# Optimization experiments

Measured on AMD Instinct MI355X. Metric: run time of the kernel, lower is better.

The kernel has to match this reference:

```python
import jax, jax.numpy as jnp
import numpy as np
from jax import lax

T, IMG, C_IN = 2048, 84, 4
HID = 256
NUM_OUT = 18
FEAT = 6 * 6 * 32  # 84 -> 42 -> 21 -> 11 -> 6 with stride-2 SAME convs


def setup_inputs() -> dict:
    key = jax.random.key(0)
    ks = jax.random.split(key, 8)
    d = {}
    d["x"] = jax.random.normal(ks[0], (T, IMG, IMG, C_IN), jnp.float32)
    cin = C_IN
    for i in range(4):
        d[f"conv_w{i}"] = jax.random.normal(ks[1 + i], (3, 3, cin, 32), jnp.float32) * (1.0 / np.sqrt(9 * cin))
        d[f"conv_b{i}"] = jnp.zeros((32,), jnp.float32)
        cin = 32
    d["lstm_w"] = jax.random.normal(ks[5], (FEAT + HID, 4 * HID), jnp.float32) * (1.0 / np.sqrt(FEAT + HID))
    d["lstm_b"] = jnp.zeros((4 * HID,), jnp.float32)
    d["fc_w"] = jax.random.normal(ks[6], (HID, NUM_OUT), jnp.float32) * 0.01
    d["fc_b"] = jnp.zeros((NUM_OUT,), jnp.float32)
    d["c_in"] = jnp.zeros((1, HID), jnp.float32)
    d["h_in"] = jnp.zeros((1, HID), jnp.float32)
    return d


def _conv_stack(x, ws, bs):
    dn = ("NHWC", "HWIO", "NHWC")
    for w, b in zip(ws, bs):
        x = jax.nn.elu(lax.conv_general_dilated(x, w, (2, 2), "SAME", dimension_numbers=dn) + b)
    return x.reshape(x.shape[0], -1)  # [T, FEAT]


def _lstm(feats, c0, h0, lstm_w, lstm_b):
    # BasicLSTMCell: gates [i, j, f, o], forget_bias = 1.0
    def step(carry, xt):
        c, h = carry  # [1, HID] each
        z = jnp.concatenate([xt[None, :], h], axis=1) @ lstm_w + lstm_b
        i, j, f, o = jnp.split(z, 4, axis=1)
        c = c * jax.nn.sigmoid(f + 1.0) + jax.nn.sigmoid(i) * jnp.tanh(j)
        h = jnp.tanh(c) * jax.nn.sigmoid(o)
        return (c, h), h[0]

    (_, _), hs = lax.scan(step, (c0, h0), feats)
    return hs  # [T, HID]


def reference(x, c_in, h_in,
              conv_w0, conv_b0, conv_w1, conv_b1,
              conv_w2, conv_b2, conv_w3, conv_b3,
              lstm_w, lstm_b, fc_w, fc_b):
    feats = _conv_stack(x, [conv_w0, conv_w1, conv_w2, conv_w3],
                        [conv_b0, conv_b1, conv_b2, conv_b3])
    hs = _lstm(feats, c_in, h_in, lstm_w, lstm_b)
    logits = hs @ fc_w + fc_b  # [T, NUM_OUT]
    return logits, hs
```

## Files before the change

kernel.cpp:

```cpp
#include <hip/hip_runtime.h>
#include <hip/hip_bf16.h>

__device__ inline float fsig(float x) { return 1.0f / (1.0f + __expf(-x)); }
__device__ inline float ftanh(float x) {
    float ax = fabsf(x);
    float e = __expf(-2.0f * ax);
    float r = (1.0f - e) / (1.0f + e);
    return x >= 0.0f ? r : -r;
}
__device__ inline float felu(float x) { return x > 0.0f ? x : expm1f(x); }

typedef _Float16 h2_t __attribute__((ext_vector_type(2)));

__device__ inline unsigned int packh2(float a, float b) {
    unsigned short ua = __builtin_bit_cast(unsigned short, (_Float16)a);
    unsigned short ub = __builtin_bit_cast(unsigned short, (_Float16)b);
    return (unsigned int)ua | ((unsigned int)ub << 16);
}
__device__ inline unsigned short f16bits(float a) {
    return __builtin_bit_cast(unsigned short, (_Float16)a);
}

__device__ inline float dot2acc(unsigned int w, unsigned int h, float acc) {
#if __has_builtin(__builtin_amdgcn_fdot2)
    return __builtin_amdgcn_fdot2(__builtin_bit_cast(h2_t, w), __builtin_bit_cast(h2_t, h), acc, false);
#else
    _Float16 wlo = __builtin_bit_cast(_Float16, (unsigned short)(w & 0xffff));
    _Float16 whi = __builtin_bit_cast(_Float16, (unsigned short)(w >> 16));
    _Float16 hlo = __builtin_bit_cast(_Float16, (unsigned short)(h & 0xffff));
    _Float16 hhi = __builtin_bit_cast(_Float16, (unsigned short)(h >> 16));
    return acc + (float)wlo * (float)hlo + (float)whi * (float)hhi;
#endif
}

template <int CIN, int W, int OW, int PAD>
__global__ __launch_bounds__(256) void conv_row(const float* __restrict__ in,
                                                const float* __restrict__ wg,
                                                const float* __restrict__ bias,
                                                float* __restrict__ out) {
    constexpr int WP = W + 2;
    __shared__ float in_s[3 * WP * CIN];
    constexpr int NQ = 3 * WP * CIN / 4;
    constexpr int QROW = WP * CIN / 4;
    const int tid = threadIdx.x;
    const int oy = blockIdx.x;
    const int t = blockIdx.y;
    const int co = tid & 31;

    for (int q = tid; q < NQ; q += 256) {
        int ky = q / QROW;
        int rem = q - ky * QROW;
        int col = rem / (CIN / 4);
        int c4 = rem - col * (CIN / 4);
        int iy = 2 * oy - PAD + ky;
        int ix = col - 1;
        float4 v = make_float4(0.f, 0.f, 0.f, 0.f);
        if (iy >= 0 && iy < W && ix >= 0 && ix < W)
            v = *(const float4*)&in[(((size_t)t * W + iy) * W + ix) * CIN + c4 * 4];
        *(float4*)&in_s[q * 4] = v;
    }

    if constexpr (CIN == 4) {
        float wr[9][4];
#pragma unroll
        for (int tap = 0; tap < 9; ++tap)
#pragma unroll
            for (int j = 0; j < 4; ++j) wr[tap][j] = wg[(tap * 4 + j) * 32 + co];
        __syncthreads();

        const int g = tid >> 5;
        constexpr int NOX = (OW + 7) / 8;
        float acc[NOX];
#pragma unroll
        for (int m = 0; m < NOX; ++m) acc[m] = 0.f;
#pragma unroll
        for (int ky = 0; ky < 3; ++ky)
#pragma unroll
            for (int kx = 0; kx < 3; ++kx) {
                float w0 = wr[ky * 3 + kx][0], w1 = wr[ky * 3 + kx][1];
                float w2 = wr[ky * 3 + kx][2], w3 = wr[ky * 3 + kx][3];
#pragma unroll
                for (int m = 0; m < NOX; ++m) {
                    int ox = g + 8 * m;
                    if (ox < OW) {
                        int cs = 2 * ox + kx - PAD + 1;
                        float4 xi = *(const float4*)&in_s[(ky * WP + cs) * 4];
                        acc[m] += xi.x * w0 + xi.y * w1 + xi.z * w2 + xi.w * w3;
                    }
                }
            }
        float b = bias[co];
#pragma unroll
        for (int m = 0; m < NOX; ++m) {
            int ox = g + 8 * m;
            if (ox < OW)
                out[(((size_t)t * OW + oy) * OW + ox) * 32 + co] = felu(acc[m] + b);
        }
    } else {
        const int cig = tid >> 5;
        float wr[9][4];
#pragma unroll
        for (int tap = 0; tap < 9; ++tap)
#pragma unroll
            for (int j = 0; j < 4; ++j) wr[tap][j] = wg[(tap * 32 + cig * 4 + j) * 32 + co];
        __syncthreads();

        float acc[OW];
#pragma unroll
        for (int ox = 0; ox < OW; ++ox) acc[ox] = 0.f;
#pragma unroll
        for (int ky = 0; ky < 3; ++ky)
#pragma unroll
            for (int kx = 0; kx < 3; ++kx) {
                const float* ip = &in_s[(ky * WP) * 32 + cig * 4];
                float w0 = wr[ky * 3 + kx][0], w1 = wr[ky * 3 + kx][1];
                float w2 = wr[ky * 3 + kx][2], w3 = wr[ky * 3 + kx][3];
#pragma unroll
                for (int ox = 0; ox < OW; ++ox) {
                    int cs = 2 * ox + kx - PAD + 1;
                    float4 xi = *(const float4*)&ip[cs * 32];
                    acc[ox] += xi.x * w0 + xi.y * w1 + xi.z * w2 + xi.w * w3;
                }
            }
        __shared__ float zs[8][OW * 32];
#pragma unroll
        for (int ox = 0; ox < OW; ++ox) zs[cig][ox * 32 + co] = acc[ox];
        __syncthreads();
        for (int idx = tid; idx < OW * 32; idx += 256) {
            float s = zs[0][idx] + zs[1][idx] + zs[2][idx] + zs[3][idx] +
                      zs[4][idx] + zs[5][idx] + zs[6][idx] + zs[7][idx] + bias[idx & 31];
            out[(((size_t)t * OW + oy) * OW) * 32 + idx] = felu(s);
        }
    }
}

__global__ void gemm_kernel(const float* __restrict__ A, const float* __restrict__ Wx,
                            const float* __restrict__ bias, float* __restrict__ C) {
    __shared__ float As[32][64];
    __shared__ float Bs[32][64];
    const int bn = blockIdx.x, bm = blockIdx.y;
    const int tx = threadIdx.x, ty = threadIdx.y;
    const int tid = ty * 16 + tx;
    float acc[4][4] = {};
    for (int k0 = 0; k0 < 1152; k0 += 32) {
        {
            int r = tid >> 3;
            int c = (tid & 7) * 4;
            float4 a0 = *(const float4*)&A[(size_t)(bm * 64 + r) * 1152 + k0 + c];
            float4 a1 = *(const float4*)&A[(size_t)(bm * 64 + r + 32) * 1152 + k0 + c];
            As[c + 0][r] = a0.x; As[c + 1][r] = a0.y; As[c + 2][r] = a0.z; As[c + 3][r] = a0.w;
            As[c + 0][r + 32] = a1.x; As[c + 1][r + 32] = a1.y; As[c + 2][r + 32] = a1.z; As[c + 3][r + 32] = a1.w;
            int rb = tid >> 4;
            int cb = (tid & 15) * 4;
            *(float4*)&Bs[rb][cb] = *(const float4*)&Wx[(size_t)(k0 + rb) * 1024 + bn * 64 + cb];
            *(float4*)&Bs[rb + 16][cb] = *(const float4*)&Wx[(size_t)(k0 + rb + 16) * 1024 + bn * 64 + cb];
        }
        __syncthreads();
#pragma unroll
        for (int kk = 0; kk < 32; ++kk) {
            float4 a = *(float4*)&As[kk][ty * 4];
            float4 b = *(float4*)&Bs[kk][tx * 4];
            acc[0][0] += a.x * b.x; acc[0][1] += a.x * b.y; acc[0][2] += a.x * b.z; acc[0][3] += a.x * b.w;
            acc[1][0] += a.y * b.x; acc[1][1] += a.y * b.y; acc[1][2] += a.y * b.z; acc[1][3] += a.y * b.w;
            acc[2][0] += a.z * b.x; acc[2][1] += a.z * b.y; acc[2][2] += a.z * b.z; acc[2][3] += a.z * b.w;
            acc[3][0] += a.w * b.x; acc[3][1] += a.w * b.y; acc[3][2] += a.w * b.z; acc[3][3] += a.w * b.w;
        }
        __syncthreads();
    }
#pragma unroll
    for (int i = 0; i < 4; ++i) {
        int row = bm * 64 + ty * 4 + i;
#pragma unroll
        for (int j = 0; j < 4; ++j) {
            int col = bn * 64 + tx * 4 + j;
            C[(size_t)row * 1024 + col] = acc[i][j] + bias[col];
        }
    }
}

__global__ __launch_bounds__(512, 2) void lstm4_kernel(const float* __restrict__ lstm_w,
                                                       const float* __restrict__ xpart,
                                                       const float* __restrict__ c_in,
                                                       const float* __restrict__ h_in,
                                                       float* __restrict__ hs_out) {
    __shared__ __align__(16) unsigned int wlds[1024][36];
    __shared__ float zsm[1024];
    __shared__ __align__(16) unsigned short hbuf[2][256];

    const int tid = threadIdx.x;
    const int c0 = tid;
    const int c1 = tid + 512;

    for (int p = 0; p < 32; ++p) {
        wlds[c0][p] = packh2(lstm_w[(size_t)(1152 + 2 * p) * 1024 + c0],
                             lstm_w[(size_t)(1152 + 2 * p + 1) * 1024 + c0]);
        wlds[c1][p] = packh2(lstm_w[(size_t)(1152 + 2 * p) * 1024 + c1],
                             lstm_w[(size_t)(1152 + 2 * p + 1) * 1024 + c1]);
    }
    unsigned int wrA[96], wrB[96];
#pragma unroll
    for (int r = 0; r < 96; ++r) {
        int p = 32 + r;
        wrA[r] = packh2(lstm_w[(size_t)(1152 + 2 * p) * 1024 + c0],
                        lstm_w[(size_t)(1152 + 2 * p + 1) * 1024 + c0]);
        wrB[r] = packh2(lstm_w[(size_t)(1152 + 2 * p) * 1024 + c1],
                        lstm_w[(size_t)(1152 + 2 * p + 1) * 1024 + c1]);
    }

    float c_state = 0.0f;
    if (tid < 256) {
        c_state = c_in[tid];
        hbuf[0][tid] = f16bits(h_in[tid]);
    }
    __syncthreads();

    float xpA = xpart[c0];
    float xpB = xpart[c1];
    for (int t = 0; t < 2048; ++t) {
        const int cur = t & 1;
        const uint4* hq = reinterpret_cast<const uint4*>(&hbuf[cur][0]);

        float a0 = 0.f, a1 = 0.f, a2 = 0.f, a3 = 0.f;
        float b0 = 0.f, b1 = 0.f, b2 = 0.f, b3 = 0.f;
#pragma unroll
        for (int c = 0; c < 8; ++c) {
            uint4 h4 = hq[c];
            uint4 wa = *reinterpret_cast<const uint4*>(&wlds[c0][4 * c]);
            uint4 wb = *reinterpret_cast<const uint4*>(&wlds[c1][4 * c]);
            a0 = dot2acc(wa.x, h4.x, a0); a1 = dot2acc(wa.y, h4.y, a1);
            a2 = dot2acc(wa.z, h4.z, a2); a3 = dot2acc(wa.w, h4.w, a3);
            b0 = dot2acc(wb.x, h4.x, b0); b1 = dot2acc(wb.y, h4.y, b1);
            b2 = dot2acc(wb.z, h4.z, b2); b3 = dot2acc(wb.w, h4.w, b3);
        }
#pragma unroll
        for (int c = 8; c < 32; ++c) {
            uint4 h4 = hq[c];
            const int r = 4 * c - 32;
            a0 = dot2acc(wrA[r + 0], h4.x, a0); a1 = dot2acc(wrA[r + 1], h4.y, a1);
            a2 = dot2acc(wrA[r + 2], h4.z, a2); a3 = dot2acc(wrA[r + 3], h4.w, a3);
            b0 = dot2acc(wrB[r + 0], h4.x, b0); b1 = dot2acc(wrB[r + 1], h4.y, b1);
            b2 = dot2acc(wrB[r + 2], h4.z, b2); b3 = dot2acc(wrB[r + 3], h4.w, b3);
        }
        zsm[c0] = (a0 + a1) + (a2 + a3) + xpA;
        zsm[c1] = (b0 + b1) + (b2 + b3) + xpB;

        float xpAn = 0.f, xpBn = 0.f;
        if (t + 1 < 2048) {
            xpAn = xpart[(size_t)(t + 1) * 1024 + c0];
            xpBn = xpart[(size_t)(t + 1) * 1024 + c1];
        }

        asm volatile("s_waitcnt lgkmcnt(0)\n\ts_barrier" ::: "memory");

        if (tid < 256) {
            float zi = zsm[tid];
            float zg = zsm[256 + tid];
            float zf = zsm[512 + tid];
            float zo = zsm[768 + tid];
            c_state = c_state * fsig(zf + 1.0f) + fsig(zi) * ftanh(zg);
            float h = ftanh(c_state) * fsig(zo);
            hs_out[(size_t)t * 256 + tid] = h;
            hbuf[cur ^ 1][tid] = f16bits(h);
        }

        asm volatile("s_waitcnt lgkmcnt(0)\n\ts_barrier" ::: "memory");
        xpA = xpAn;
        xpB = xpBn;
    }
}

__global__ void logits_kernel(const float* __restrict__ hs, const float* __restrict__ fc_w,
                              const float* __restrict__ fc_b, float* __restrict__ out) {
    int idx = blockIdx.x * 256 + threadIdx.x;
    if (idx >= 2048 * 18) return;
    int t = idx / 18, n = idx % 18;
    float acc = fc_b[n];
    const float* hrow = hs + (size_t)t * 256;
#pragma unroll 4
    for (int k = 0; k < 256; ++k) acc += hrow[k] * fc_w[k * 18 + n];
    out[idx] = acc;
}

extern "C" void kernel_launch(void* const* d_in, const int* in_sizes, int n_in,
                              void* d_out, int out_size, void* d_ws, size_t ws_size,
                              hipStream_t stream) {
    const float* x   = (const float*)d_in[0];
    const float* w0  = (const float*)d_in[1];
    const float* b0  = (const float*)d_in[2];
    const float* w1  = (const float*)d_in[3];
    const float* b1  = (const float*)d_in[4];
    const float* w2  = (const float*)d_in[5];
    const float* b2  = (const float*)d_in[6];
    const float* w3  = (const float*)d_in[7];
    const float* b3  = (const float*)d_in[8];
    const float* lw  = (const float*)d_in[9];
    const float* lb  = (const float*)d_in[10];
    const float* fcw = (const float*)d_in[11];
    const float* fcb = (const float*)d_in[12];
    const float* cin = (const float*)d_in[13];
    const float* hin = (const float*)d_in[14];

    float* outp = (float*)d_out;
    float* hs_out = outp + 2048 * 18;

    const size_t PERT = 56448 + 14112 + 3872;
    const size_t FIXED = (size_t)2048 * 1152 + (size_t)2048 * 1024;

    int C = 128;
    const int cands[4] = {2048, 1024, 512, 256};
    for (int i = 0; i < 4; ++i) {
        if ((FIXED + (size_t)cands[i] * PERT) * 4 <= ws_size) { C = cands[i]; break; }
    }

    float* ws    = (float*)d_ws;
    float* c0buf = ws;
    float* c1buf = c0buf + (size_t)C * 56448;
    float* c2buf = c1buf + (size_t)C * 14112;
    float* feats = c2buf + (size_t)C * 3872;
    float* xpart = feats + (size_t)2048 * 1152;

    for (int t0 = 0; t0 < 2048; t0 += C) {
        const float* xin = x + (size_t)t0 * 84 * 84 * 4;
        conv_row<4, 84, 42, 0><<<dim3(42, C), 256, 0, stream>>>(xin, w0, b0, c0buf);
        conv_row<32, 42, 21, 0><<<dim3(21, C), 256, 0, stream>>>(c0buf, w1, b1, c1buf);
        conv_row<32, 21, 11, 1><<<dim3(11, C), 256, 0, stream>>>(c1buf, w2, b2, c2buf);
        conv_row<32, 11, 6, 1><<<dim3(6, C), 256, 0, stream>>>(c2buf, w3, b3,
                                                               feats + (size_t)t0 * 1152);
    }

    gemm_kernel<<<dim3(16, 32), dim3(16, 16), 0, stream>>>(feats, lw, lb, xpart);
    lstm4_kernel<<<1, 512, 0, stream>>>(lw, xpart, cin, hin, hs_out);
    logits_kernel<<<144, 256, 0, stream>>>(hs_out, fcw, fcb, outp);
}
```

Baseline: 4.672 ms.

## Store conv intermediates in fp16 and use packed fdot2 for conv layers 1-3

Conv activations between layers are now stored as fp16 instead of fp32, which halves the intermediate memory traffic and workspace use, so larger time chunks fit. Conv layers 1-3 now use packed half2 dot products (fdot2) with fp16-packed weights and split the output columns across two thread halves, with 4 channel groups instead of 8. This lowers shared-memory traffic and ALU work, at the cost of fp16 rounding of activations and weights, which may affect accuracy.

Result: faster. 4.561 ms (-2.4%).

```diff
diff --git a/kernel.cpp b/kernel.cpp
--- a/kernel.cpp
+++ b/kernel.cpp
@@ -33,104 +33,142 @@
 #endif
 }
 
-template <int CIN, int W, int OW, int PAD>
-__global__ __launch_bounds__(256) void conv_row(const float* __restrict__ in,
-                                                const float* __restrict__ wg,
-                                                const float* __restrict__ bias,
-                                                float* __restrict__ out) {
-    constexpr int WP = W + 2;
-    __shared__ float in_s[3 * WP * CIN];
-    constexpr int NQ = 3 * WP * CIN / 4;
-    constexpr int QROW = WP * CIN / 4;
+__global__ __launch_bounds__(256) void conv0_kernel(const float* __restrict__ in,
+                                                    const float* __restrict__ wg,
+                                                    const float* __restrict__ bias,
+                                                    unsigned short* __restrict__ out) {
+    constexpr int W = 84, OW = 42, PAD = 0, WP = W + 2;
+    __shared__ float in_s[3 * WP * 4];
+    constexpr int NQ = 3 * WP;
     const int tid = threadIdx.x;
     const int oy = blockIdx.x;
     const int t = blockIdx.y;
     const int co = tid & 31;
 
     for (int q = tid; q < NQ; q += 256) {
-        int ky = q / QROW;
-        int rem = q - ky * QROW;
-        int col = rem / (CIN / 4);
-        int c4 = rem - col * (CIN / 4);
+        int ky = q / WP;
+        int col = q - ky * WP;
         int iy = 2 * oy - PAD + ky;
         int ix = col - 1;
         float4 v = make_float4(0.f, 0.f, 0.f, 0.f);
         if (iy >= 0 && iy < W && ix >= 0 && ix < W)
-            v = *(const float4*)&in[(((size_t)t * W + iy) * W + ix) * CIN + c4 * 4];
+            v = *(const float4*)&in[(((size_t)t * W + iy) * W + ix) * 4];
         *(float4*)&in_s[q * 4] = v;
     }
 
-    if constexpr (CIN == 4) {
-        float wr[9][4];
-#pragma unroll
-        for (int tap = 0; tap < 9; ++tap)
-#pragma unroll
-            for (int j = 0; j < 4; ++j) wr[tap][j] = wg[(tap * 4 + j) * 32 + co];
-        __syncthreads();
-
-        const int g = tid >> 5;
-        constexpr int NOX = (OW + 7) / 8;
-        float acc[NOX];
-#pragma unroll
-        for (int m = 0; m < NOX; ++m) acc[m] = 0.f;
-#pragma unroll
-        for (int ky = 0; ky < 3; ++ky)
-#pragma unroll
-            for (int kx = 0; kx < 3; ++kx) {
-                float w0 = wr[ky * 3 + kx][0], w1 = wr[ky * 3 + kx][1];
-                float w2 = wr[ky * 3 + kx][2], w3 = wr[ky * 3 + kx][3];
-#pragma unroll
-                for (int m = 0; m < NOX; ++m) {
-                    int ox = g + 8 * m;
-                    if (ox < OW) {
-                        int cs = 2 * ox + kx - PAD + 1;
-                        float4 xi = *(const float4*)&in_s[(ky * WP + cs) * 4];
-                        acc[m] += xi.x * w0 + xi.y * w1 + xi.z * w2 + xi.w * w3;
-                    }
+    float wr[9][4];
+#pragma unroll
+    for (int tap = 0; tap < 9; ++tap)
+#pragma unroll
+        for (int j = 0; j < 4; ++j) wr[tap][j] = wg[(tap * 4 + j) * 32 + co];
+    __syncthreads();
+
+    const int g = tid >> 5;
+    constexpr int NOX = (OW + 7) / 8;
+    float acc[NOX];
+#pragma unroll
+    for (int m = 0; m < NOX; ++m) acc[m] = 0.f;
+#pragma unroll
+    for (int ky = 0; ky < 3; ++ky)
+#pragma unroll
+        for (int kx = 0; kx < 3; ++kx) {
+            float w0 = wr[ky * 3 + kx][0], w1 = wr[ky * 3 + kx][1];
+            float w2 = wr[ky * 3 + kx][2], w3 = wr[ky * 3 + kx][3];
+#pragma unroll
+            for (int m = 0; m < NOX; ++m) {
+                int ox = g + 8 * m;
+                if (ox < OW) {
+                    int cs = 2 * ox + kx - PAD + 1;
+                    float4 xi = *(const float4*)&in_s[(ky * WP + cs) * 4];
+                    acc[m] += xi.x * w0 + xi.y * w1 + xi.z * w2 + xi.w * w3;
                 }
             }
-        float b = bias[co];
-#pragma unroll
-        for (int m = 0; m < NOX; ++m) {
-            int ox = g + 8 * m;
-            if (ox < OW)
-                out[(((size_t)t * OW + oy) * OW + ox) * 32 + co] = felu(acc[m] + b);
-        }
-    } else {
-        const int cig = tid >> 5;
-        float wr[9][4];
-#pragma unroll
-        for (int tap = 0; tap < 9; ++tap)
-#pragma unroll
-            for (int j = 0; j < 4; ++j) wr[tap][j] = wg[(tap * 32 + cig * 4 + j) * 32 + co];
-        __syncthreads();
-
-        float acc[OW];
-#pragma unroll
-        for (int ox = 0; ox < OW; ++ox) acc[ox] = 0.f;
-#pragma unroll
-        for (int ky = 0; ky < 3; ++ky)
-#pragma unroll
-            for (int kx = 0; kx < 3; ++kx) {
-                const float* ip = &in_s[(ky * WP) * 32 + cig * 4];
-                float w0 = wr[ky * 3 + kx][0], w1 = wr[ky * 3 + kx][1];
-                float w2 = wr[ky * 3 + kx][2], w3 = wr[ky * 3 + kx][3];
-#pragma unroll
-                for (int ox = 0; ox < OW; ++ox) {
+        }
+    float b = bias[co];
+#pragma unroll
+    for (int m = 0; m < NOX; ++m) {
+        int ox = g + 8 * m;
+        if (ox < OW)
+            out[(((size_t)t * OW + oy) * OW + ox) * 32 + co] = f16bits(felu(acc[m] + b));
+    }
+}
+
+template <int W, int OW, int PAD, bool F32OUT>
+__global__ __launch_bounds__(256) void convh_kernel(const unsigned short* __restrict__ in,
+                                                    const float* __restrict__ wg,
+                                                    const float* __restrict__ bias,
+                                                    void* __restrict__ outv) {
+    constexpr int WP = W + 2;
+    constexpr int OWH = (OW + 1) / 2;
+    __shared__ __align__(16) unsigned short in_s[3][WP][32];
+    __shared__ float zs[4][OW * 32];
+
+    const int tid = threadIdx.x;
+    const int oy = blockIdx.x;
+    const int t = blockIdx.y;
+    const int co = tid & 31;
+    const int cig = (tid >> 5) & 3;
+    const int oxh = tid >> 7;
+
+    constexpr int NQ4 = 3 * WP * 4;
+    uint4* in_s4 = reinterpret_cast<uint4*>(&in_s[0][0][0]);
+    for (int q = tid; q < NQ4; q += 256) {
+        int ky = q / (WP * 4);
+        int rem = q - ky * (WP * 4);
+        int col = rem >> 2, c4 = rem & 3;
+        int iy = 2 * oy - PAD + ky;
+        int ix = col - 1;
+        uint4 v = make_uint4(0u, 0u, 0u, 0u);
+        if (iy >= 0 && iy < W && ix >= 0 && ix < W)
+            v = *(const uint4*)&in[(((size_t)t * W + iy) * W + ix) * 32 + c4 * 8];
+        in_s4[q] = v;
+    }
+
+    unsigned int wr[9][4];
+#pragma unroll
+    for (int tap = 0; tap < 9; ++tap)
+#pragma unroll
+        for (int p = 0; p < 4; ++p)
+            wr[tap][p] = packh2(wg[(tap * 32 + cig * 8 + 2 * p) * 32 + co],
+                                wg[(tap * 32 + cig * 8 + 2 * p + 1) * 32 + co]);
+    __syncthreads();
+
+    float acc[OWH];
+#pragma unroll
+    for (int m = 0; m < OWH; ++m) acc[m] = 0.f;
+#pragma unroll
+    for (int ky = 0; ky < 3; ++ky)
+#pragma unroll
+        for (int kx = 0; kx < 3; ++kx) {
+            unsigned int w0 = wr[ky * 3 + kx][0], w1 = wr[ky * 3 + kx][1];
+            unsigned int w2 = wr[ky * 3 + kx][2], w3 = wr[ky * 3 + kx][3];
+#pragma unroll
+            for (int m = 0; m < OWH; ++m) {
+                int ox = oxh * OWH + m;
+                if (ox < OW) {
                     int cs = 2 * ox + kx - PAD + 1;
-                    float4 xi = *(const float4*)&ip[cs * 32];
-                    acc[ox] += xi.x * w0 + xi.y * w1 + xi.z * w2 + xi.w * w3;
+                    uint4 h8 = *(const uint4*)&in_s[ky][cs][cig * 8];
+                    acc[m] = dot2acc(w0, h8.x, acc[m]);
+                    acc[m] = dot2acc(w1, h8.y, acc[m]);
+                    acc[m] = dot2acc(w2, h8.z, acc[m]);
+                    acc[m] = dot2acc(w3, h8.w, acc[m]);
                 }
             }
-        __shared__ float zs[8][OW * 32];
-#pragma unroll
-        for (int ox = 0; ox < OW; ++ox) zs[cig][ox * 32 + co] = acc[ox];
-        __syncthreads();
-        for (int idx = tid; idx < OW * 32; idx += 256) {
-            float s = zs[0][idx] + zs[1][idx] + zs[2][idx] + zs[3][idx] +
-                      zs[4][idx] + zs[5][idx] + zs[6][idx] + zs[7][idx] + bias[idx & 31];
-            out[(((size_t)t * OW + oy) * OW) * 32 + idx] = felu(s);
-        }
+        }
+#pragma unroll
+    for (int m = 0; m < OWH; ++m) {
+        int ox = oxh * OWH + m;
+        if (ox < OW) zs[cig][ox * 32 + co] = acc[m];
+    }
+    __syncthreads();
+
+    for (int idx = tid; idx < OW * 32; idx += 256) {
+        float s = zs[0][idx] + zs[1][idx] + zs[2][idx] + zs[3][idx] + bias[idx & 31];
+        s = felu(s);
+        if constexpr (F32OUT)
+            ((float*)outv)[(((size_t)t * OW + oy) * OW) * 32 + idx] = s;
+        else
+            ((unsigned short*)outv)[(((size_t)t * OW + oy) * OW) * 32 + idx] = f16bits(s);
     }
 }
 
@@ -303,29 +341,28 @@
     float* outp = (float*)d_out;
     float* hs_out = outp + 2048 * 18;
 
-    const size_t PERT = 56448 + 14112 + 3872;
-    const size_t FIXED = (size_t)2048 * 1152 + (size_t)2048 * 1024;
+    const size_t FIXED_B = ((size_t)2048 * 1152 + (size_t)2048 * 1024) * 4;
+    const size_t PERT_B = ((size_t)56448 + 14112 + 3872) * 2;
 
     int C = 128;
-    const int cands[4] = {2048, 1024, 512, 256};
-    for (int i = 0; i < 4; ++i) {
-        if ((FIXED + (size_t)cands[i] * PERT) * 4 <= ws_size) { C = cands[i]; break; }
-    }
-
-    float* ws    = (float*)d_ws;
-    float* c0buf = ws;
-    float* c1buf = c0buf + (size_t)C * 56448;
-    float* c2buf = c1buf + (size_t)C * 14112;
-    float* feats = c2buf + (size_t)C * 3872;
+    const int cands[5] = {2048, 1024, 512, 256, 128};
+    for (int i = 0; i < 5; ++i) {
+        if (FIXED_B + (size_t)cands[i] * PERT_B <= ws_size) { C = cands[i]; break; }
+    }
+
+    float* feats = (float*)d_ws;
     float* xpart = feats + (size_t)2048 * 1152;
+    unsigned short* c0buf = (unsigned short*)(xpart + (size_t)2048 * 1024);
+    unsigned short* c1buf = c0buf + (size_t)C * 56448;
+    unsigned short* c2buf = c1buf + (size_t)C * 14112;
 
     for (int t0 = 0; t0 < 2048; t0 += C) {
         const float* xin = x + (size_t)t0 * 84 * 84 * 4;
-        conv_row<4, 84, 42, 0><<<dim3(42, C), 256, 0, stream>>>(xin, w0, b0, c0buf);
-        conv_row<32, 42, 21, 0><<<dim3(21, C), 256, 0, stream>>>(c0buf, w1, b1, c1buf);
-        conv_row<32, 21, 11, 1><<<dim3(11, C), 256, 0, stream>>>(c1buf, w2, b2, c2buf);
-        conv_row<32, 11, 6, 1><<<dim3(6, C), 256, 0, stream>>>(c2buf, w3, b3,
-                                                               feats + (size_t)t0 * 1152);
+        conv0_kernel<<<dim3(42, C), 256, 0, stream>>>(xin, w0, b0, c0buf);
+        convh_kernel<42, 21, 0, false><<<dim3(21, C), 256, 0, stream>>>(c0buf, w1, b1, c1buf);
+        convh_kernel<21, 11, 1, false><<<dim3(11, C), 256, 0, stream>>>(c1buf, w2, b2, c2buf);
+        convh_kernel<11, 6, 1, true><<<dim3(6, C), 256, 0, stream>>>(c2buf, w3, b3,
+                                                                     feats + (size_t)t0 * 1152);
     }
 
     gemm_kernel<<<dim3(16, 32), dim3(16, 16), 0, stream>>>(feats, lw, lb, xpart);
```
